# Kernel optimization log

Measured on AMD Instinct MI355X. Metric: run time of the kernel, lower is better.

## Reference

```python
import jax, jax.numpy as jnp
import numpy as np

H = 128  # hidden width


def _mlp(xy, W0, b0, W1, b1, W2, b2, W3, b3):
    # xy: [..., 2] -> [..., 1], tanh MLP
    h = jnp.tanh(xy @ W0 + b0)
    h = jnp.tanh(h @ W1 + b1)
    h = jnp.tanh(h @ W2 + b2)
    return h @ W3 + b3


def setup_inputs() -> dict:
    key = jax.random.key(0)
    ks = jax.random.split(key, 8)
    n_int, n_bd = 262144, 16384
    inp = {
        "xy_int": jax.random.uniform(ks[0], (n_int, 2), dtype=jnp.float32),
        "f": jax.random.normal(ks[1], (n_int, 1), dtype=jnp.float32),
        "xy_bd": jax.random.uniform(ks[2], (n_bd, 2), dtype=jnp.float32),
        "g": jax.random.normal(ks[3], (n_bd, 1), dtype=jnp.float32),
        # Glorot-ish scaled weights
        "W0": jax.random.normal(ks[4], (2, H), dtype=jnp.float32) / np.sqrt(2.0),
        "b0": jnp.zeros((H,), jnp.float32),
        "W1": jax.random.normal(ks[5], (H, H), dtype=jnp.float32) / np.sqrt(H),
        "b1": jnp.zeros((H,), jnp.float32),
        "W2": jax.random.normal(ks[6], (H, H), dtype=jnp.float32) / np.sqrt(H),
        "b2": jnp.zeros((H,), jnp.float32),
        "W3": jax.random.normal(ks[7], (H, 1), dtype=jnp.float32) / np.sqrt(H),
        "b3": jnp.zeros((1,), jnp.float32),
    }
    return inp


def reference(xy_int, f, xy_bd, g, W0, b0, W1, b1, W2, b2, W3, b3):
    params = (W0, b0, W1, b1, W2, b2, W3, b3)
    n_int = xy_int.shape[0]
    n_bd = xy_bd.shape[0]

    # boundary loss: 0.5/n_bd * ||u(xy_bd) - g||^2
    pred_bd = _mlp(xy_bd, *params)
    diff_bd = pred_bd.reshape(-1) - g.reshape(-1)
    loss_bound = 0.5 / n_bd * jnp.sum(diff_bd * diff_bd)

    # interior PDE residual: u_xx + u_yy (Laplacian) per collocation point
    def u_scalar(p):  # p: [2] -> scalar
        return _mlp(p[None, :], *params)[0, 0]

    def lap_point(p):
        return jnp.trace(jax.hessian(u_scalar)(p))  # 2x2 Hessian trace

    pred_f = jax.vmap(lap_point)(xy_int)  # [n_int]
    diff_f = pred_f.reshape(-1) - f.reshape(-1)
    loss_f = 0.5 / n_int * jnp.sum(diff_f * diff_f)

    return (loss_bound, loss_f)
```

## Files before the change

kernel.cpp:

```cpp
#include <hip/hip_runtime.h>

#define HID 128
#define PTS 32
#define KP  136
#define FRAGS_PER_W 2048
#define WS_ELEMS (FRAGS_PER_W * 8)

typedef float v4f  __attribute__((ext_vector_type(4)));
typedef float v16f __attribute__((ext_vector_type(16)));
typedef short s8v  __attribute__((ext_vector_type(8)));

__device__ __forceinline__ unsigned short f2bf(float f) {
    unsigned u = __builtin_bit_cast(unsigned, f);
    u = (u + 0x7FFFu + ((u >> 16) & 1u)) >> 16;
    return (unsigned short)u;
}
__device__ __forceinline__ float bf2f(unsigned short h) {
    unsigned u = ((unsigned)h) << 16;
    return __builtin_bit_cast(float, u);
}

#if __has_builtin(__builtin_amdgcn_cvt_pk_bf16_f32)
typedef __bf16 bf16x2 __attribute__((ext_vector_type(2)));
__device__ __forceinline__ unsigned pk2(float f0, float f1) {
    return __builtin_bit_cast(unsigned, __builtin_amdgcn_cvt_pk_bf16_f32(f0, f1));
}
#else
__device__ __forceinline__ unsigned pk2(float f0, float f1) {
    unsigned u0 = __builtin_bit_cast(unsigned, f0);
    unsigned u1 = __builtin_bit_cast(unsigned, f1);
    u0 += 0x7FFFu + ((u0 >> 16) & 1u);
    u1 += 0x7FFFu + ((u1 >> 16) & 1u);
    return __builtin_amdgcn_perm(u1, u0, 0x07060302u);
}
#endif
__device__ __forceinline__ uint2 pk4(const float* f) {
    uint2 h;
    h.x = pk2(f[0], f[1]);
    h.y = pk2(f[2], f[3]);
    return h;
}

__device__ __forceinline__ float fast_tanh(float x) {
#if __has_builtin(__builtin_amdgcn_exp2f)
    float e = __builtin_amdgcn_exp2f(x * 2.885390081777927f);
#else
    float e = __expf(2.0f * x);
#endif
    float r = __builtin_amdgcn_rcpf(e + 1.0f);
    return 1.0f - 2.0f * r;
}

__global__ __launch_bounds__(256) void prep_w_kernel(
    const float* __restrict__ W1, const float* __restrict__ W2,
    unsigned short* __restrict__ ws, float* __restrict__ out)
{
    if (blockIdx.x == 0 && threadIdx.x < 2) out[threadIdx.x] = 0.0f;
    const int t = blockIdx.x * 256 + threadIdx.x;
    const int w = t >> 11;
    const int r = t & 2047;
    const int mw = r >> 9;
    const int ks8 = (r >> 6) & 7;
    const int lane = r & 63;
    const int m = mw * 32 + (lane & 31);
    const int kb = ks8 * 16 + (lane >> 5) * 8;
    const float* W = w ? W2 : W1;
    s8v hv, lv;
    #pragma unroll
    for (int i = 0; i < 8; ++i) {
        float f = W[(kb + i) * HID + m];
        unsigned short hh = f2bf(f);
        hv[i] = (short)hh;
        lv[i] = (short)f2bf(f - bf2f(hh));
    }
    *(s8v*)&ws[((size_t)(w * 2 + 0) * FRAGS_PER_W + r) * 8] = hv;
    *(s8v*)&ws[((size_t)(w * 2 + 1) * FRAGS_PER_W + r) * 8] = lv;
}

__global__ __launch_bounds__(256, 4) void pinn_mfma_kernel(
    const float* __restrict__ xy_int, const float* __restrict__ f_t,
    const float* __restrict__ xy_bd, const float* __restrict__ g_t,
    const float* __restrict__ W0, const float* __restrict__ b0,
    const float* __restrict__ b1, const float* __restrict__ b2,
    const float* __restrict__ W3, const float* __restrict__ b3,
    const unsigned short* __restrict__ ws, float* __restrict__ out,
    int gi, float scale_int, float scale_bd)
{
    extern __shared__ char smem_raw[];
    unsigned short* sBh = (unsigned short*)smem_raw;
    float* sRed = (float*)(sBh + 4 * 32 * KP);

    const bool is_bd = (int)blockIdx.x >= gi;
    const float* __restrict__ xy  = is_bd ? xy_bd : xy_int;
    const float* __restrict__ tgt = is_bd ? g_t : f_t;
    const int rc = is_bd ? 0 : 3;
    const int pbase = (is_bd ? ((int)blockIdx.x - gi) : (int)blockIdx.x) * PTS;

    const int tid  = threadIdx.x;
    const int lane = tid & 63;
    const int mw   = tid >> 6;
    const int l31  = lane & 31;
    const int kh   = lane >> 5;

    {
        const int tj = tid & 31, tp = tid >> 5;
        const int j0 = tj * 4, p0 = tp * 4;
        float wx[4], wy[4], bb[4];
        #pragma unroll
        for (int jj = 0; jj < 4; ++jj) {
            wx[jj] = W0[j0 + jj];
            wy[jj] = W0[HID + j0 + jj];
            bb[jj] = b0[j0 + jj];
        }
        #pragma unroll
        for (int pp = 0; pp < 4; ++pp) {
            const int p = p0 + pp;
            const float2 t2 = ((const float2*)xy)[pbase + p];
            float chv[4][4];
            #pragma unroll
            for (int jj = 0; jj < 4; ++jj) {
                float z = fmaf(t2.x, wx[jj], fmaf(t2.y, wy[jj], bb[jj]));
                float a = fast_tanh(z);
                float t = fmaf(-a, a, 1.0f);
                float s2 = fmaf(wx[jj], wx[jj], wy[jj] * wy[jj]);
                chv[0][jj] = a;
                chv[1][jj] = t * wx[jj];
                chv[2][jj] = t * wy[jj];
                chv[3][jj] = -2.0f * a * t * s2;
            }
            #pragma unroll
            for (int c = 0; c < 4; ++c) {
                const int row = (c * 32 + p) * KP + j0;
                *(uint2*)&sBh[row] = pk4(chv[c]);
            }
        }
    }
    __syncthreads();

    #pragma unroll
    for (int L = 0; L < 2; ++L) {
        const unsigned short* wshi = ws + (size_t)L * 2 * WS_ELEMS;
        const unsigned short* wslo = wshi + WS_ELEMS;

        s8v whi[2][2], wlo[2][2];
        #pragma unroll
        for (int h = 0; h < 2; ++h) {
            const int idx = mw * 512 + h * 64 + lane;
            whi[0][h] = *(const s8v*)&wshi[(size_t)idx * 8];
            wlo[0][h] = *(const s8v*)&wslo[(size_t)idx * 8];
        }

        v16f acc[4] = {};

        #pragma unroll
        for (int s = 0; s < 4; ++s) {
            const int cur = s & 1, nxt = cur ^ 1;
            if (s < 3) {
                #pragma unroll
                for (int h = 0; h < 2; ++h) {
                    const int idx = mw * 512 + ((s + 1) * 2 + h) * 64 + lane;
                    whi[nxt][h] = *(const s8v*)&wshi[(size_t)idx * 8];
                    wlo[nxt][h] = *(const s8v*)&wslo[(size_t)idx * 8];
                }
            }
            #pragma unroll
            for (int h = 0; h < 2; ++h) {
                const int koff = (s * 2 + h) * 16 + kh * 8;
                #pragma unroll
                for (int nt = 0; nt < 4; ++nt) {
                    s8v bh = *(const s8v*)&sBh[(nt * 32 + l31) * KP + koff];
                    acc[nt] = __builtin_amdgcn_mfma_f32_32x32x16_bf16(
                        whi[cur][h], bh, acc[nt], 0, 0, 0);
                    acc[nt] = __builtin_amdgcn_mfma_f32_32x32x16_bf16(
                        wlo[cur][h], bh, acc[nt], 0, 0, 0);
                }
            }
        }
        __syncthreads();

        const float* __restrict__ bptr = (L == 0) ? b1 : b2;
        #pragma unroll
        for (int g = 0; g < 4; ++g) {
            const int j0g = mw * 32 + 8 * g + 4 * kh;
            const v4f bb = *(const v4f*)&bptr[j0g];
            float chv[4][4];
            #pragma unroll
            for (int r = 0; r < 4; ++r) {
                float z = acc[0][g * 4 + r] + bb[r];
                float a = fast_tanh(z);
                float t = fmaf(-a, a, 1.0f);
                float zx = acc[1][g * 4 + r], zy = acc[2][g * 4 + r],
                      zl = acc[3][g * 4 + r];
                float s2 = fmaf(zx, zx, zy * zy);
                chv[0][r] = a;
                chv[1][r] = t * zx;
                chv[2][r] = t * zy;
                chv[3][r] = fmaf(t, zl, -2.0f * a * t * s2);
            }
            #pragma unroll
            for (int c = 0; c < 4; ++c) {
                if (L == 1 && c != rc) continue;
                const int row = (c * 32 + l31) * KP + j0g;
                *(uint2*)&sBh[row] = pk4(chv[c]);
            }
        }
        __syncthreads();
    }

    {
        const int p  = tid >> 3;
        const int i  = tid & 7;
        const int k0 = i * 16;
        const int row = (rc * 32 + p) * KP + k0;
        float r = 0.0f;
        #pragma unroll
        for (int h = 0; h < 2; ++h) {
            s8v vh = *(const s8v*)&sBh[row + h * 8];
            #pragma unroll
            for (int t = 0; t < 8; ++t)
                r = fmaf(bf2f((unsigned short)vh[t]), W3[k0 + h * 8 + t], r);
        }
        r += __shfl_xor(r, 1, 64);
        r += __shfl_xor(r, 2, 64);
        r += __shfl_xor(r, 4, 64);
        if (i == 0) {
            float d = r + (is_bd ? b3[0] : 0.0f) - tgt[pbase + p];
            sRed[p] = d * d;
        }
    }
    __syncthreads();
    if (tid == 0) {
        float s = 0.0f;
        #pragma unroll
        for (int p = 0; p < PTS; ++p) s += sRed[p];
        atomicAdd(out + (is_bd ? 0 : 1), s * (is_bd ? scale_bd : scale_int));
    }
}

extern "C" void kernel_launch(void* const* d_in, const int* in_sizes, int n_in,
                              void* d_out, int out_size, void* d_ws, size_t ws_size,
                              hipStream_t stream) {
    const float* xy_int = (const float*)d_in[0];
    const float* f      = (const float*)d_in[1];
    const float* xy_bd  = (const float*)d_in[2];
    const float* g      = (const float*)d_in[3];
    const float* W0 = (const float*)d_in[4];
    const float* b0 = (const float*)d_in[5];
    const float* W1 = (const float*)d_in[6];
    const float* b1 = (const float*)d_in[7];
    const float* W2 = (const float*)d_in[8];
    const float* b2 = (const float*)d_in[9];
    const float* W3 = (const float*)d_in[10];
    const float* b3 = (const float*)d_in[11];
    float* out = (float*)d_out;
    unsigned short* ws = (unsigned short*)d_ws;

    const int n_int = in_sizes[0] / 2;
    const int n_bd  = in_sizes[2] / 2;

    prep_w_kernel<<<16, 256, 0, stream>>>(W1, W2, ws, out);

    const int smem = (4 * 32 * KP) * 2 + PTS * 4;
    const int gi = n_int / PTS;
    const int gb = n_bd / PTS;

    pinn_mfma_kernel<<<gi + gb, 256, smem, stream>>>(
        xy_int, f, xy_bd, g, W0, b0, b1, b2, W3, b3, ws, out,
        gi, 0.5f / (float)n_int, 0.5f / (float)n_bd);
}
```

Baseline: 215.6 us.

## Skip derivative channels for boundary blocks and fuse output layer into epilogue

Boundary blocks only need the forward value, so they now compute and store only channel 0 and run a single MFMA tile per step instead of four. The final layer no longer writes activations back to shared memory: the tanh, Laplacian combination and W3 dot product are done directly from accumulators in fp32, reduced across waves through a small shared buffer, and then through wave shuffles. This removes a shared-memory round trip, one barrier and a bf16 rounding step. It adds divergent code paths keyed on block type.

```diff
diff --git a/kernel.cpp b/kernel.cpp
--- a/kernel.cpp
+++ b/kernel.cpp
@@ -88,12 +88,11 @@
 {
     extern __shared__ char smem_raw[];
     unsigned short* sBh = (unsigned short*)smem_raw;
-    float* sRed = (float*)(sBh + 4 * 32 * KP);
+    float* sPart = (float*)(sBh + 4 * 32 * KP);
 
     const bool is_bd = (int)blockIdx.x >= gi;
     const float* __restrict__ xy  = is_bd ? xy_bd : xy_int;
     const float* __restrict__ tgt = is_bd ? g_t : f_t;
-    const int rc = is_bd ? 0 : 3;
     const int pbase = (is_bd ? ((int)blockIdx.x - gi) : (int)blockIdx.x) * PTS;
 
     const int tid  = threadIdx.x;
@@ -121,21 +120,26 @@
             for (int jj = 0; jj < 4; ++jj) {
                 float z = fmaf(t2.x, wx[jj], fmaf(t2.y, wy[jj], bb[jj]));
                 float a = fast_tanh(z);
-                float t = fmaf(-a, a, 1.0f);
-                float s2 = fmaf(wx[jj], wx[jj], wy[jj] * wy[jj]);
                 chv[0][jj] = a;
-                chv[1][jj] = t * wx[jj];
-                chv[2][jj] = t * wy[jj];
-                chv[3][jj] = -2.0f * a * t * s2;
-            }
-            #pragma unroll
-            for (int c = 0; c < 4; ++c) {
-                const int row = (c * 32 + p) * KP + j0;
-                *(uint2*)&sBh[row] = pk4(chv[c]);
+                if (!is_bd) {
+                    float t = fmaf(-a, a, 1.0f);
+                    float s2 = fmaf(wx[jj], wx[jj], wy[jj] * wy[jj]);
+                    chv[1][jj] = t * wx[jj];
+                    chv[2][jj] = t * wy[jj];
+                    chv[3][jj] = -2.0f * a * t * s2;
+                }
+            }
+            *(uint2*)&sBh[(0 * 32 + p) * KP + j0] = pk4(chv[0]);
+            if (!is_bd) {
+                #pragma unroll
+                for (int c = 1; c < 4; ++c)
+                    *(uint2*)&sBh[(c * 32 + p) * KP + j0] = pk4(chv[c]);
             }
         }
     }
     __syncthreads();
+
+    v16f acc[4];
 
     #pragma unroll
     for (int L = 0; L < 2; ++L) {
@@ -150,7 +154,8 @@
             wlo[0][h] = *(const s8v*)&wslo[(size_t)idx * 8];
         }
 
-        v16f acc[4] = {};
+        #pragma unroll
+        for (int nt = 0; nt < 4; ++nt) acc[nt] = (v16f)0.0f;
 
         #pragma unroll
         for (int s = 0; s < 4; ++s) {
@@ -166,74 +171,101 @@
             #pragma unroll
             for (int h = 0; h < 2; ++h) {
                 const int koff = (s * 2 + h) * 16 + kh * 8;
+                if (is_bd) {
+                    s8v bh = *(const s8v*)&sBh[l31 * KP + koff];
+                    acc[0] = __builtin_amdgcn_mfma_f32_32x32x16_bf16(
+                        whi[cur][h], bh, acc[0], 0, 0, 0);
+                    acc[0] = __builtin_amdgcn_mfma_f32_32x32x16_bf16(
+                        wlo[cur][h], bh, acc[0], 0, 0, 0);
+                } else {
+                    #pragma unroll
+                    for (int nt = 0; nt < 4; ++nt) {
+                        s8v bh = *(const s8v*)&sBh[(nt * 32 + l31) * KP + koff];
+                        acc[nt] = __builtin_amdgcn_mfma_f32_32x32x16_bf16(
+                            whi[cur][h], bh, acc[nt], 0, 0, 0);
+                        acc[nt] = __builtin_amdgcn_mfma_f32_32x32x16_bf16(
+                            wlo[cur][h], bh, acc[nt], 0, 0, 0);
+                    }
+                }
+            }
+        }
+
+        if (L == 0) {
+            __syncthreads();
+            #pragma unroll
+            for (int g = 0; g < 4; ++g) {
+                const int j0g = mw * 32 + 8 * g + 4 * kh;
+                const v4f bb = *(const v4f*)&b1[j0g];
+                float chv[4][4];
                 #pragma unroll
-                for (int nt = 0; nt < 4; ++nt) {
-                    s8v bh = *(const s8v*)&sBh[(nt * 32 + l31) * KP + koff];
-                    acc[nt] = __builtin_amdgcn_mfma_f32_32x32x16_bf16(
-                        whi[cur][h], bh, acc[nt], 0, 0, 0);
-                    acc[nt] = __builtin_amdgcn_mfma_f32_32x32x16_bf16(
-                        wlo[cur][h], bh, acc[nt], 0, 0, 0);
-                }
-            }
-        }
-        __syncthreads();
-
-        const float* __restrict__ bptr = (L == 0) ? b1 : b2;
+                for (int r = 0; r < 4; ++r) {
+                    float z = acc[0][g * 4 + r] + bb[r];
+                    float a = fast_tanh(z);
+                    chv[0][r] = a;
+                    if (!is_bd) {
+                        float t = fmaf(-a, a, 1.0f);
+                        float zx = acc[1][g * 4 + r], zy = acc[2][g * 4 + r],
+                              zl = acc[3][g * 4 + r];
+                        float s2 = fmaf(zx, zx, zy * zy);
+                        chv[1][r] = t * zx;
+                        chv[2][r] = t * zy;
+                        chv[3][r] = fmaf(t, zl, -2.0f * a * t * s2);
+                    }
+                }
+                *(uint2*)&sBh[(0 * 32 + l31) * KP + j0g] = pk4(chv[0]);
+                if (!is_bd) {
+                    #pragma unroll
+                    for (int c = 1; c < 4; ++c)
+                        *(uint2*)&sBh[(c * 32 + l31) * KP + j0g] = pk4(chv[c]);
+                }
+            }
+            __syncthreads();
+        }
+    }
+
+    {
+        float part = 0.0f;
         #pragma unroll
         for (int g = 0; g < 4; ++g) {
             const int j0g = mw * 32 + 8 * g + 4 * kh;
-            const v4f bb = *(const v4f*)&bptr[j0g];
-            float chv[4][4];
+            const v4f bb = *(const v4f*)&b2[j0g];
+            const v4f w3 = *(const v4f*)&W3[j0g];
             #pragma unroll
             for (int r = 0; r < 4; ++r) {
                 float z = acc[0][g * 4 + r] + bb[r];
                 float a = fast_tanh(z);
-                float t = fmaf(-a, a, 1.0f);
-                float zx = acc[1][g * 4 + r], zy = acc[2][g * 4 + r],
-                      zl = acc[3][g * 4 + r];
-                float s2 = fmaf(zx, zx, zy * zy);
-                chv[0][r] = a;
-                chv[1][r] = t * zx;
-                chv[2][r] = t * zy;
-                chv[3][r] = fmaf(t, zl, -2.0f * a * t * s2);
-            }
-            #pragma unroll
-            for (int c = 0; c < 4; ++c) {
-                if (L == 1 && c != rc) continue;
-                const int row = (c * 32 + l31) * KP + j0g;
-                *(uint2*)&sBh[row] = pk4(chv[c]);
-            }
-        }
+                float v;
+                if (is_bd) {
+                    v = a;
+                } else {
+                    float t = fmaf(-a, a, 1.0f);
+                    float zx = acc[1][g * 4 + r], zy = acc[2][g * 4 + r],
+                          zl = acc[3][g * 4 + r];
+                    float s2 = fmaf(zx, zx, zy * zy);
+                    v = t * fmaf(-2.0f * a, s2, zl);
+                }
+                part = fmaf(v, w3[r], part);
+            }
+        }
+        part += __shfl_xor(part, 32, 64);
+        if (kh == 0) sPart[mw * 32 + l31] = part;
         __syncthreads();
-    }
-
-    {
-        const int p  = tid >> 3;
-        const int i  = tid & 7;
-        const int k0 = i * 16;
-        const int row = (rc * 32 + p) * KP + k0;
-        float r = 0.0f;
-        #pragma unroll
-        for (int h = 0; h < 2; ++h) {
-            s8v vh = *(const s8v*)&sBh[row + h * 8];
-            #pragma unroll
-            for (int t = 0; t < 8; ++t)
-                r = fmaf(bf2f((unsigned short)vh[t]), W3[k0 + h * 8 + t], r);
-        }
-        r += __shfl_xor(r, 1, 64);
-        r += __shfl_xor(r, 2, 64);
-        r += __shfl_xor(r, 4, 64);
-        if (i == 0) {
-            float d = r + (is_bd ? b3[0] : 0.0f) - tgt[pbase + p];
-            sRed[p] = d * d;
-        }
-    }
-    __syncthreads();
-    if (tid == 0) {
-        float s = 0.0f;
-        #pragma unroll
-        for (int p = 0; p < PTS; ++p) s += sRed[p];
-        atomicAdd(out + (is_bd ? 0 : 1), s * (is_bd ? scale_bd : scale_int));
+        if (mw == 0) {
+            const int p = l31;
+            float pred = (sPart[p] + sPart[32 + p]) + (sPart[64 + p] + sPart[96 + p])
+                       + (is_bd ? b3[0] : 0.0f);
+            float d = pred - tgt[pbase + p];
+            float sq = (kh == 0) ? d * d : 0.0f;
+            sq += __shfl_xor(sq, 1, 64);
+            sq += __shfl_xor(sq, 2, 64);
+            sq += __shfl_xor(sq, 4, 64);
+            sq += __shfl_xor(sq, 8, 64);
+            sq += __shfl_xor(sq, 16, 64);
+            sq += __shfl_xor(sq, 32, 64);
+            if (lane == 0)
+                atomicAdd(out + (is_bd ? 0 : 1),
+                          sq * (is_bd ? scale_bd : scale_int));
+        }
     }
 }
 
@@ -260,7 +292,7 @@
 
     prep_w_kernel<<<16, 256, 0, stream>>>(W1, W2, ws, out);
 
-    const int smem = (4 * 32 * KP) * 2 + PTS * 4;
+    const int smem = (4 * 32 * KP) * 2 + 128 * 4;
     const int gi = n_int / PTS;
     const int gb = n_bd / PTS;
 
```

Measured after the change: 254.5 us. 18.1% more time.
